# Performance work log

Measured on AMD Instinct MI355X. Metric: run time of the kernel, lower is better.

Reference implementation:

```python
import jax, jax.numpy as jnp
import numpy as np

B, S, D = 4, 2048, 1024

def setup_inputs() -> dict:
    key = jax.random.key(0)
    k0, k1, k2, k3, k4, k5 = jax.random.split(key, 6)
    scale = 1.0 / np.sqrt(D)
    return {
        "input_seq_embs": jax.random.normal(k0, (B, S, D), dtype=jnp.float32),
        "W_Q": jax.random.normal(k1, (D, D), dtype=jnp.float32) * scale,
        "W_K": jax.random.normal(k2, (D, D), dtype=jnp.float32) * scale,
        "W_V": jax.random.normal(k3, (D, D), dtype=jnp.float32) * scale,
        "W_O": jax.random.normal(k4, (D, D), dtype=jnp.float32) * scale,
        "b_O": jax.random.normal(k5, (D,), dtype=jnp.float32) * 0.01,
    }

def reference(input_seq_embs, W_Q, W_K, W_V, W_O, b_O):
    # torch nn.Linear: y = x @ W.T
    Q = jnp.einsum('bsd,ed->bse', input_seq_embs, W_Q)
    K = jnp.einsum('bsd,ed->bse', input_seq_embs, W_K)
    V = jnp.einsum('bsd,ed->bse', input_seq_embs, W_V)
    # NOTE: no 1/sqrt(d) scaling in the original module
    A = jnp.einsum('bqd,bkd->bqk', Q, K)  # [B,S,S]
    # log(tril(ones)) == 0 on/below diagonal, -inf above
    causal = jnp.tril(jnp.ones((S, S), dtype=bool))
    A = jnp.where(causal[None, :, :], A, -jnp.inf)
    A = jax.nn.softmax(A, axis=-1)
    # dropout layers are identity in eval mode
    out = jnp.einsum('bqk,bkd->bqd', A, V)
    out = jnp.einsum('bsd,ed->bse', out, W_O) + b_O
    return out
```

## Files before the change

kernel.cpp:

```cpp
#include <hip/hip_runtime.h>
#include <cstdint>

typedef _Float16 f16x8 __attribute__((ext_vector_type(8)));
typedef _Float16 f16x4 __attribute__((ext_vector_type(4)));
typedef float    f32x4 __attribute__((ext_vector_type(4)));

#define AS1 __attribute__((address_space(1)))
#define AS3 __attribute__((address_space(3)))

__device__ __forceinline__ void load16_lds(const void* g, void* l) {
  __builtin_amdgcn_global_load_lds((AS1 void*)g, (AS3 void*)l, 16, 0, 0);
}

__global__ __launch_bounds__(256) void cvt_all(
    const float* __restrict__ x, const float* __restrict__ wq,
    const float* __restrict__ wk, const float* __restrict__ wv,
    const float* __restrict__ wo,
    _Float16* __restrict__ xh, _Float16* __restrict__ wcat,
    _Float16* __restrict__ woh) {
  long long g = (long long)blockIdx.x * 256 + threadIdx.x;
  const float* in; _Float16* out; long long idx;
  if (g < 2097152)      { in = x;  out = xh;             idx = g; }
  else if (g < 2359296) { in = wq; out = wcat;           idx = g - 2097152; }
  else if (g < 2621440) { in = wk; out = wcat + 1048576; idx = g - 2359296; }
  else if (g < 2883584) { in = wv; out = wcat + 2097152; idx = g - 2621440; }
  else                  { in = wo; out = woh;            idx = g - 2883584; }
  float4 v = ((const float4*)in)[idx];
  f16x4 o;
  o[0] = (_Float16)v.x; o[1] = (_Float16)v.y; o[2] = (_Float16)v.z; o[3] = (_Float16)v.w;
  ((f16x4*)out)[idx] = o;
}

__global__ __launch_bounds__(256) void softmax_causal(float* __restrict__ Sbuf) {
  int g = blockIdx.x;
  int row = g & 2047;
  float* srow = Sbuf + (size_t)g * 2048;
  _Float16* prow = (_Float16*)srow + 2048;
  int L = row + 1;
  int L4 = L & ~3;
  int Lp = ((row >> 7) + 1) << 7;
  int t = threadIdx.x;
  int lane = t & 63, w = t >> 6;

  const float4* s4 = (const float4*)srow;
  float4 v[2];
  int cnt = 0;
  float mx = -3.0e38f;
  for (int j4 = t; j4 * 4 < L4; j4 += 256) {
    float4 q = s4[j4];
    v[cnt++] = q;
    mx = fmaxf(mx, fmaxf(fmaxf(q.x, q.y), fmaxf(q.z, q.w)));
  }
  int jt = L4 + t;
  float tailv = 0.f;
  bool hasTail = (jt < L);
  if (hasTail) { tailv = srow[jt]; mx = fmaxf(mx, tailv); }

  __shared__ float sm[8];
  #pragma unroll
  for (int off = 32; off > 0; off >>= 1) mx = fmaxf(mx, __shfl_down(mx, off));
  if (lane == 0) sm[w] = mx;
  __syncthreads();
  if (t == 0) { float m2 = sm[0]; for (int q = 1; q < 4; q++) m2 = fmaxf(m2, sm[q]); sm[0] = m2; }
  __syncthreads();
  mx = sm[0];

  float sum = 0.f;
  for (int c = 0; c < cnt; c++) {
    v[c].x = __expf(v[c].x - mx); v[c].y = __expf(v[c].y - mx);
    v[c].z = __expf(v[c].z - mx); v[c].w = __expf(v[c].w - mx);
    sum += (v[c].x + v[c].y) + (v[c].z + v[c].w);
  }
  float te = 0.f;
  if (hasTail) { te = __expf(tailv - mx); sum += te; }
  #pragma unroll
  for (int off = 32; off > 0; off >>= 1) sum += __shfl_down(sum, off);
  if (lane == 0) sm[4 + w] = sum;
  __syncthreads();
  if (t == 0) sm[4] = 1.0f / (sm[4] + sm[5] + sm[6] + sm[7]);
  __syncthreads();
  float inv = sm[4];

  f16x4* p4 = (f16x4*)prow;
  cnt = 0;
  for (int j4 = t; j4 * 4 < L4; j4 += 256) {
    float4 q = v[cnt++];
    f16x4 o;
    o[0] = (_Float16)(q.x * inv); o[1] = (_Float16)(q.y * inv);
    o[2] = (_Float16)(q.z * inv); o[3] = (_Float16)(q.w * inv);
    p4[j4] = o;
  }
  if (hasTail) prow[jt] = (_Float16)(te * inv);
  for (int j = L + t; j < Lp; j += 256) prow[j] = (_Float16)0.0f;
}

template <int OUTMODE, bool CAUSAL_SKIP>
__global__ __launch_bounds__(256) void gemm_bt(
    const _Float16* __restrict__ A, const _Float16* __restrict__ B,
    void* __restrict__ Cv, const float* __restrict__ bias,
    int K, int lda, int ldb, int ldc,
    long long aBatch, long long bBatch, long long cBatch) {
  int bx = blockIdx.x, by = blockIdx.y, bz = blockIdx.z;
  if (CAUSAL_SKIP && bx > by) return;
  const _Float16* Ab = A + (long long)bz * aBatch + (long long)by * 128 * lda;
  const _Float16* Bb = B + (long long)bz * bBatch + (long long)bx * 128 * ldb;

  __shared__ _Float16 lA[128 * 32];
  __shared__ _Float16 lB[128 * 32];

  int tid = threadIdx.x;
  int r0 = tid >> 2;
  int c0 = (tid & 3) * 8;
  const _Float16* ga0 = Ab + (long long)r0 * lda + c0;
  const _Float16* ga1 = Ab + (long long)(r0 + 64) * lda + c0;
  const _Float16* gb0 = Bb + (long long)r0 * ldb + c0;
  const _Float16* gb1 = Bb + (long long)(r0 + 64) * ldb + c0;
  _Float16* la0 = lA + tid * 8;
  _Float16* la1 = lA + 2048 + tid * 8;
  _Float16* lb0 = lB + tid * 8;
  _Float16* lb1 = lB + 2048 + tid * 8;

  f32x4 acc[4][4] = {};
  int lane = tid & 63;
  int wv = tid >> 6;
  int wm = (wv & 1) * 64, wn = (wv >> 1) * 64;
  int l16 = lane & 15, quad = lane >> 4;
  const _Float16* raBase = lA + (wm + l16) * 32 + quad * 8;
  const _Float16* rbBase = lB + (wn + l16) * 32 + quad * 8;

  for (int kb = 0; kb < K; kb += 32) {
    __syncthreads();
    load16_lds(ga0, la0);
    load16_lds(ga1, la1);
    load16_lds(gb0, lb0);
    load16_lds(gb1, lb1);
    ga0 += 32; ga1 += 32; gb0 += 32; gb1 += 32;
    __syncthreads();
    f16x8 af[4], bfr[4];
    #pragma unroll
    for (int i = 0; i < 4; i++) af[i] = *(const f16x8*)(raBase + i * 512);
    #pragma unroll
    for (int j = 0; j < 4; j++) bfr[j] = *(const f16x8*)(rbBase + j * 512);
    #pragma unroll
    for (int i = 0; i < 4; i++)
      #pragma unroll
      for (int j = 0; j < 4; j++)
        acc[i][j] = __builtin_amdgcn_mfma_f32_16x16x32_f16(af[i], bfr[j], acc[i][j], 0, 0, 0);
  }

  int m0 = by * 128 + wm + quad * 4;
  int n0 = bx * 128 + wn + l16;

  if (OUTMODE == 2) {
    float* C = (float*)Cv + (long long)bz * cBatch;
    #pragma unroll
    for (int i = 0; i < 4; i++)
      #pragma unroll
      for (int j = 0; j < 4; j++)
        #pragma unroll
        for (int r = 0; r < 4; r++)
          C[(long long)(m0 + i * 16 + r) * ldc + (n0 + j * 16)] = acc[i][j][r];
  } else {
    float* C = (float*)Cv + (long long)bz * cBatch;
    #pragma unroll
    for (int j = 0; j < 4; j++) {
      float bj = bias[n0 + j * 16];
      #pragma unroll
      for (int i = 0; i < 4; i++)
        #pragma unroll
        for (int r = 0; r < 4; r++)
          C[(long long)(m0 + i * 16 + r) * ldc + (n0 + j * 16)] = acc[i][j][r] + bj;
    }
  }
}

__global__ __launch_bounds__(256) void qkv_gemm(
    const _Float16* __restrict__ A, const _Float16* __restrict__ B,
    _Float16* __restrict__ Qh, _Float16* __restrict__ Kh, _Float16* __restrict__ Vt) {
  int bx = blockIdx.x, by = blockIdx.y;
  const _Float16* Ab = A + (long long)by * 128 * 1024;
  const _Float16* Bb = B + (long long)bx * 128 * 1024;

  __shared__ _Float16 lA[128 * 32];
  __shared__ _Float16 lB[128 * 32];

  int tid = threadIdx.x;
  int r0 = tid >> 2;
  int c0 = (tid & 3) * 8;
  const _Float16* ga0 = Ab + (long long)r0 * 1024 + c0;
  const _Float16* ga1 = Ab + (long long)(r0 + 64) * 1024 + c0;
  const _Float16* gb0 = Bb + (long long)r0 * 1024 + c0;
  const _Float16* gb1 = Bb + (long long)(r0 + 64) * 1024 + c0;
  _Float16* la0 = lA + tid * 8;
  _Float16* la1 = lA + 2048 + tid * 8;
  _Float16* lb0 = lB + tid * 8;
  _Float16* lb1 = lB + 2048 + tid * 8;

  f32x4 acc[4][4] = {};
  int lane = tid & 63;
  int wv = tid >> 6;
  int wm = (wv & 1) * 64, wn = (wv >> 1) * 64;
  int l16 = lane & 15, quad = lane >> 4;
  const _Float16* raBase = lA + (wm + l16) * 32 + quad * 8;
  const _Float16* rbBase = lB + (wn + l16) * 32 + quad * 8;

  for (int kb = 0; kb < 1024; kb += 32) {
    __syncthreads();
    load16_lds(ga0, la0);
    load16_lds(ga1, la1);
    load16_lds(gb0, lb0);
    load16_lds(gb1, lb1);
    ga0 += 32; ga1 += 32; gb0 += 32; gb1 += 32;
    __syncthreads();
    f16x8 af[4], bfr[4];
    #pragma unroll
    for (int i = 0; i < 4; i++) af[i] = *(const f16x8*)(raBase + i * 512);
    #pragma unroll
    for (int j = 0; j < 4; j++) bfr[j] = *(const f16x8*)(rbBase + j * 512);
    #pragma unroll
    for (int i = 0; i < 4; i++)
      #pragma unroll
      for (int j = 0; j < 4; j++)
        acc[i][j] = __builtin_amdgcn_mfma_f32_16x16x32_f16(af[i], bfr[j], acc[i][j], 0, 0, 0);
  }

  int m0 = by * 128 + wm + quad * 4;
  int n0 = bx * 128 + wn + l16;

  if (bx < 16) {
    _Float16* C = (bx < 8) ? Qh : Kh;
    int nr = n0 & 1023;
    #pragma unroll
    for (int i = 0; i < 4; i++)
      #pragma unroll
      for (int j = 0; j < 4; j++)
        #pragma unroll
        for (int r = 0; r < 4; r++)
          C[(long long)(m0 + i * 16 + r) * 1024 + (nr + j * 16)] = (_Float16)acc[i][j][r];
  } else {
    int d0 = n0 - 2048;
    #pragma unroll
    for (int i = 0; i < 4; i++) {
      long long mm = m0 + i * 16;
      long long b = mm >> 11;
      long long s = mm & 2047;
      #pragma unroll
      for (int j = 0; j < 4; j++) {
        f16x4 pk;
        #pragma unroll
        for (int r = 0; r < 4; r++) pk[r] = (_Float16)acc[i][j][r];
        *(f16x4*)(Vt + (b << 21) + (long long)(d0 + j * 16) * 2048 + s) = pk;
      }
    }
  }
}

__global__ __launch_bounds__(256) void pv_splitk(
    const _Float16* __restrict__ P,
    const _Float16* __restrict__ Vt,
    float* __restrict__ P0, float* __restrict__ P1,
    _Float16* __restrict__ Oh) {
  int bx = blockIdx.x, cy = blockIdx.y, bz = blockIdx.z;
  int by, c;
  if (cy < 8) { by = cy; c = 0; }
  else { int q = cy - 8; by = 8 + (q >> 1); c = q & 1; }
  int kmax = (by + 1) * 128;
  int k0 = c * 1024;
  int klen = min(kmax, k0 + 1024) - k0;

  const _Float16* Ab = P + (long long)bz * 8388608LL + (long long)by * 128 * 4096 + k0;
  const _Float16* Bb = Vt + (long long)bz * 2097152LL + (long long)bx * 128 * 2048 + k0;

  __shared__ _Float16 lA[128 * 32];
  __shared__ _Float16 lB[128 * 32];

  int tid = threadIdx.x;
  int r0 = tid >> 2;
  int c0 = (tid & 3) * 8;
  const _Float16* ga0 = Ab + (long long)r0 * 4096 + c0;
  const _Float16* ga1 = Ab + (long long)(r0 + 64) * 4096 + c0;
  const _Float16* gb0 = Bb + (long long)r0 * 2048 + c0;
  const _Float16* gb1 = Bb + (long long)(r0 + 64) * 2048 + c0;
  _Float16* la0 = lA + tid * 8;
  _Float16* la1 = lA + 2048 + tid * 8;
  _Float16* lb0 = lB + tid * 8;
  _Float16* lb1 = lB + 2048 + tid * 8;

  f32x4 acc[4][4] = {};
  int lane = tid & 63;
  int wv = tid >> 6;
  int wm = (wv & 1) * 64, wn = (wv >> 1) * 64;
  int l16 = lane & 15, quad = lane >> 4;
  const _Float16* raBase = lA + (wm + l16) * 32 + quad * 8;
  const _Float16* rbBase = lB + (wn + l16) * 32 + quad * 8;

  for (int kb = 0; kb < klen; kb += 32) {
    __syncthreads();
    load16_lds(ga0, la0);
    load16_lds(ga1, la1);
    load16_lds(gb0, lb0);
    load16_lds(gb1, lb1);
    ga0 += 32; ga1 += 32; gb0 += 32; gb1 += 32;
    __syncthreads();
    f16x8 af[4], bfr[4];
    #pragma unroll
    for (int i = 0; i < 4; i++) af[i] = *(const f16x8*)(raBase + i * 512);
    #pragma unroll
    for (int j = 0; j < 4; j++) bfr[j] = *(const f16x8*)(rbBase + j * 512);
    #pragma unroll
    for (int i = 0; i < 4; i++)
      #pragma unroll
      for (int j = 0; j < 4; j++)
        acc[i][j] = __builtin_amdgcn_mfma_f32_16x16x32_f16(af[i], bfr[j], acc[i][j], 0, 0, 0);
  }

  int m0 = by * 128 + wm + quad * 4;
  int n0 = bx * 128 + wn + l16;

  if (c == 0 && by < 8) {
    _Float16* C = Oh + (long long)bz * 2097152LL;
    #pragma unroll
    for (int i = 0; i < 4; i++)
      #pragma unroll
      for (int j = 0; j < 4; j++)
        #pragma unroll
        for (int r = 0; r < 4; r++)
          C[(long long)(m0 + i * 16 + r) * 1024 + (n0 + j * 16)] = (_Float16)acc[i][j][r];
  } else if (c == 0) {
    float* C = P0 + (long long)bz * 2097152LL;
    #pragma unroll
    for (int i = 0; i < 4; i++)
      #pragma unroll
      for (int j = 0; j < 4; j++)
        #pragma unroll
        for (int r = 0; r < 4; r++)
          C[(long long)(m0 + i * 16 + r) * 1024 + (n0 + j * 16)] = acc[i][j][r];
  } else {
    float* C = P1 + (long long)bz * 1048576LL;
    int mr = m0 - 1024;
    #pragma unroll
    for (int i = 0; i < 4; i++)
      #pragma unroll
      for (int j = 0; j < 4; j++)
        #pragma unroll
        for (int r = 0; r < 4; r++)
          C[(long long)(mr + i * 16 + r) * 1024 + (n0 + j * 16)] = acc[i][j][r];
  }
}

__global__ __launch_bounds__(256) void pv_reduce(const float* __restrict__ P0,
                                                 const float* __restrict__ P1,
                                                 _Float16* __restrict__ Oh) {
  int i = blockIdx.x * 256 + threadIdx.x;
  if (i >= 1048576) return;
  int f4 = i;
  int bz = f4 >> 18;
  int loc = f4 & 262143;
  long long p0i = (long long)bz * 524288 + 262144 + loc;
  float4 v = ((const float4*)P0)[p0i];
  float4 w = ((const float4*)P1)[f4];
  v.x += w.x; v.y += w.y; v.z += w.z; v.w += w.w;
  f16x4 o;
  o[0] = (_Float16)v.x; o[1] = (_Float16)v.y; o[2] = (_Float16)v.z; o[3] = (_Float16)v.w;
  ((f16x4*)Oh)[p0i] = o;
}


extern "C" void kernel_launch(void* const* d_in, const int* in_sizes, int n_in,
                              void* d_out, int out_size, void* d_ws, size_t ws_size,
                              hipStream_t stream) {
  const float* x  = (const float*)d_in[0];
  const float* Wq = (const float*)d_in[1];
  const float* Wk = (const float*)d_in[2];
  const float* Wv = (const float*)d_in[3];
  const float* Wo = (const float*)d_in[4];
  const float* bO = (const float*)d_in[5];

  char* ws = (char*)d_ws;
  _Float16* xh   = (_Float16*)(ws + 0);
  _Float16* Wcat = (_Float16*)(ws + 16777216);
  _Float16* Woh  = (_Float16*)(ws + 23068672);
  _Float16* Qh   = (_Float16*)(ws + 25165824);
  _Float16* Kh   = (_Float16*)(ws + 41943040);
  _Float16* Vt   = (_Float16*)(ws + 58720256);
  _Float16* Oh   = (_Float16*)(ws + 75497472);
  float*    Sb   = (float*)   (ws + 92274688);
  float*    P0   = (float*)   (ws + 25165824);
  float*    P1   = (float*)   (ws + 0);

  dim3 blk(256);

  cvt_all<<<12288, blk, 0, stream>>>(x, Wq, Wk, Wv, Wo, xh, Wcat, Woh);

  qkv_gemm<<<dim3(24, 64, 1), blk, 0, stream>>>(xh, Wcat, Qh, Kh, Vt);

  gemm_bt<2, true><<<dim3(16, 16, 4), blk, 0, stream>>>(
      Qh, Kh, Sb, nullptr, 1024, 1024, 1024, 2048,
      2097152LL, 2097152LL, 4194304LL);

  softmax_causal<<<8192, blk, 0, stream>>>(Sb);

  pv_splitk<<<dim3(8, 24, 4), blk, 0, stream>>>(
      (const _Float16*)Sb + 2048, Vt, P0, P1, Oh);
  pv_reduce<<<4096, blk, 0, stream>>>(P0, P1, Oh);

  gemm_bt<3, false><<<dim3(8, 64, 1), blk, 0, stream>>>(
      Oh, Woh, (float*)d_out, bO, 1024, 1024, 1024, 1024, 0, 0, 0);
}
```

Before: 340.3 us.

## Fuse per-tile softmax stats into scores GEMM and store fp16 scores

The scores GEMM now computes per-tile row max and exp-sum in its epilogue, writes fp16 max-shifted scores plus per-tile (max, sum) stats, and a lighter normalize pass rescales the scores into probabilities in place. This replaces the fp32 score buffer and the full-row softmax kernel, cutting the score traffic from fp32 to fp16 and removing the separate max/sum reduction passes. The trade-offs are extra epilogue work and shared-memory reductions in the GEMM, plus precision loss from storing shifted scores in fp16 before exponentiation. The generic gemm_bt template is split into a dedicated output-projection kernel.

```diff
diff --git a/kernel.cpp b/kernel.cpp
--- a/kernel.cpp
+++ b/kernel.cpp
@@ -31,149 +31,6 @@
   ((f16x4*)out)[idx] = o;
 }
 
-__global__ __launch_bounds__(256) void softmax_causal(float* __restrict__ Sbuf) {
-  int g = blockIdx.x;
-  int row = g & 2047;
-  float* srow = Sbuf + (size_t)g * 2048;
-  _Float16* prow = (_Float16*)srow + 2048;
-  int L = row + 1;
-  int L4 = L & ~3;
-  int Lp = ((row >> 7) + 1) << 7;
-  int t = threadIdx.x;
-  int lane = t & 63, w = t >> 6;
-
-  const float4* s4 = (const float4*)srow;
-  float4 v[2];
-  int cnt = 0;
-  float mx = -3.0e38f;
-  for (int j4 = t; j4 * 4 < L4; j4 += 256) {
-    float4 q = s4[j4];
-    v[cnt++] = q;
-    mx = fmaxf(mx, fmaxf(fmaxf(q.x, q.y), fmaxf(q.z, q.w)));
-  }
-  int jt = L4 + t;
-  float tailv = 0.f;
-  bool hasTail = (jt < L);
-  if (hasTail) { tailv = srow[jt]; mx = fmaxf(mx, tailv); }
-
-  __shared__ float sm[8];
-  #pragma unroll
-  for (int off = 32; off > 0; off >>= 1) mx = fmaxf(mx, __shfl_down(mx, off));
-  if (lane == 0) sm[w] = mx;
-  __syncthreads();
-  if (t == 0) { float m2 = sm[0]; for (int q = 1; q < 4; q++) m2 = fmaxf(m2, sm[q]); sm[0] = m2; }
-  __syncthreads();
-  mx = sm[0];
-
-  float sum = 0.f;
-  for (int c = 0; c < cnt; c++) {
-    v[c].x = __expf(v[c].x - mx); v[c].y = __expf(v[c].y - mx);
-    v[c].z = __expf(v[c].z - mx); v[c].w = __expf(v[c].w - mx);
-    sum += (v[c].x + v[c].y) + (v[c].z + v[c].w);
-  }
-  float te = 0.f;
-  if (hasTail) { te = __expf(tailv - mx); sum += te; }
-  #pragma unroll
-  for (int off = 32; off > 0; off >>= 1) sum += __shfl_down(sum, off);
-  if (lane == 0) sm[4 + w] = sum;
-  __syncthreads();
-  if (t == 0) sm[4] = 1.0f / (sm[4] + sm[5] + sm[6] + sm[7]);
-  __syncthreads();
-  float inv = sm[4];
-
-  f16x4* p4 = (f16x4*)prow;
-  cnt = 0;
-  for (int j4 = t; j4 * 4 < L4; j4 += 256) {
-    float4 q = v[cnt++];
-    f16x4 o;
-    o[0] = (_Float16)(q.x * inv); o[1] = (_Float16)(q.y * inv);
-    o[2] = (_Float16)(q.z * inv); o[3] = (_Float16)(q.w * inv);
-    p4[j4] = o;
-  }
-  if (hasTail) prow[jt] = (_Float16)(te * inv);
-  for (int j = L + t; j < Lp; j += 256) prow[j] = (_Float16)0.0f;
-}
-
-template <int OUTMODE, bool CAUSAL_SKIP>
-__global__ __launch_bounds__(256) void gemm_bt(
-    const _Float16* __restrict__ A, const _Float16* __restrict__ B,
-    void* __restrict__ Cv, const float* __restrict__ bias,
-    int K, int lda, int ldb, int ldc,
-    long long aBatch, long long bBatch, long long cBatch) {
-  int bx = blockIdx.x, by = blockIdx.y, bz = blockIdx.z;
-  if (CAUSAL_SKIP && bx > by) return;
-  const _Float16* Ab = A + (long long)bz * aBatch + (long long)by * 128 * lda;
-  const _Float16* Bb = B + (long long)bz * bBatch + (long long)bx * 128 * ldb;
-
-  __shared__ _Float16 lA[128 * 32];
-  __shared__ _Float16 lB[128 * 32];
-
-  int tid = threadIdx.x;
-  int r0 = tid >> 2;
-  int c0 = (tid & 3) * 8;
-  const _Float16* ga0 = Ab + (long long)r0 * lda + c0;
-  const _Float16* ga1 = Ab + (long long)(r0 + 64) * lda + c0;
-  const _Float16* gb0 = Bb + (long long)r0 * ldb + c0;
-  const _Float16* gb1 = Bb + (long long)(r0 + 64) * ldb + c0;
-  _Float16* la0 = lA + tid * 8;
-  _Float16* la1 = lA + 2048 + tid * 8;
-  _Float16* lb0 = lB + tid * 8;
-  _Float16* lb1 = lB + 2048 + tid * 8;
-
-  f32x4 acc[4][4] = {};
-  int lane = tid & 63;
-  int wv = tid >> 6;
-  int wm = (wv & 1) * 64, wn = (wv >> 1) * 64;
-  int l16 = lane & 15, quad = lane >> 4;
-  const _Float16* raBase = lA + (wm + l16) * 32 + quad * 8;
-  const _Float16* rbBase = lB + (wn + l16) * 32 + quad * 8;
-
-  for (int kb = 0; kb < K; kb += 32) {
-    __syncthreads();
-    load16_lds(ga0, la0);
-    load16_lds(ga1, la1);
-    load16_lds(gb0, lb0);
-    load16_lds(gb1, lb1);
-    ga0 += 32; ga1 += 32; gb0 += 32; gb1 += 32;
-    __syncthreads();
-    f16x8 af[4], bfr[4];
-    #pragma unroll
-    for (int i = 0; i < 4; i++) af[i] = *(const f16x8*)(raBase + i * 512);
-    #pragma unroll
-    for (int j = 0; j < 4; j++) bfr[j] = *(const f16x8*)(rbBase + j * 512);
-    #pragma unroll
-    for (int i = 0; i < 4; i++)
-      #pragma unroll
-      for (int j = 0; j < 4; j++)
-        acc[i][j] = __builtin_amdgcn_mfma_f32_16x16x32_f16(af[i], bfr[j], acc[i][j], 0, 0, 0);
-  }
-
-  int m0 = by * 128 + wm + quad * 4;
-  int n0 = bx * 128 + wn + l16;
-
-  if (OUTMODE == 2) {
-    float* C = (float*)Cv + (long long)bz * cBatch;
-    #pragma unroll
-    for (int i = 0; i < 4; i++)
-      #pragma unroll
-      for (int j = 0; j < 4; j++)
-        #pragma unroll
-        for (int r = 0; r < 4; r++)
-          C[(long long)(m0 + i * 16 + r) * ldc + (n0 + j * 16)] = acc[i][j][r];
-  } else {
-    float* C = (float*)Cv + (long long)bz * cBatch;
-    #pragma unroll
-    for (int j = 0; j < 4; j++) {
-      float bj = bias[n0 + j * 16];
-      #pragma unroll
-      for (int i = 0; i < 4; i++)
-        #pragma unroll
-        for (int r = 0; r < 4; r++)
-          C[(long long)(m0 + i * 16 + r) * ldc + (n0 + j * 16)] = acc[i][j][r] + bj;
-    }
-  }
-}
-
 __global__ __launch_bounds__(256) void qkv_gemm(
     const _Float16* __restrict__ A, const _Float16* __restrict__ B,
     _Float16* __restrict__ Qh, _Float16* __restrict__ Kh, _Float16* __restrict__ Vt) {
@@ -252,6 +109,195 @@
         *(f16x4*)(Vt + (b << 21) + (long long)(d0 + j * 16) * 2048 + s) = pk;
       }
     }
+  }
+}
+
+__global__ __launch_bounds__(256) void scores_gemm(
+    const _Float16* __restrict__ Qh, const _Float16* __restrict__ Kh,
+    _Float16* __restrict__ S, float2* __restrict__ stats) {
+  int bx = blockIdx.x, by = blockIdx.y, bz = blockIdx.z;
+  if (bx > by) return;
+  const _Float16* Ab = Qh + (long long)bz * 2097152 + (long long)by * 128 * 1024;
+  const _Float16* Bb = Kh + (long long)bz * 2097152 + (long long)bx * 128 * 1024;
+
+  __shared__ _Float16 lA[128 * 32];
+  __shared__ _Float16 lB[128 * 32];
+  __shared__ float redM[128];
+  __shared__ float redL[128];
+
+  int tid = threadIdx.x;
+  int r0 = tid >> 2;
+  int c0 = (tid & 3) * 8;
+  const _Float16* ga0 = Ab + (long long)r0 * 1024 + c0;
+  const _Float16* ga1 = Ab + (long long)(r0 + 64) * 1024 + c0;
+  const _Float16* gb0 = Bb + (long long)r0 * 1024 + c0;
+  const _Float16* gb1 = Bb + (long long)(r0 + 64) * 1024 + c0;
+  _Float16* la0 = lA + tid * 8;
+  _Float16* la1 = lA + 2048 + tid * 8;
+  _Float16* lb0 = lB + tid * 8;
+  _Float16* lb1 = lB + 2048 + tid * 8;
+
+  f32x4 acc[4][4] = {};
+  int lane = tid & 63;
+  int wv = tid >> 6;
+  int wm = (wv & 1) * 64, wn = (wv >> 1) * 64;
+  int l16 = lane & 15, quad = lane >> 4;
+  const _Float16* raBase = lA + (wm + l16) * 32 + quad * 8;
+  const _Float16* rbBase = lB + (wn + l16) * 32 + quad * 8;
+
+  for (int kb = 0; kb < 1024; kb += 32) {
+    __syncthreads();
+    load16_lds(ga0, la0);
+    load16_lds(ga1, la1);
+    load16_lds(gb0, lb0);
+    load16_lds(gb1, lb1);
+    ga0 += 32; ga1 += 32; gb0 += 32; gb1 += 32;
+    __syncthreads();
+    f16x8 af[4], bfr[4];
+    #pragma unroll
+    for (int i = 0; i < 4; i++) af[i] = *(const f16x8*)(raBase + i * 512);
+    #pragma unroll
+    for (int j = 0; j < 4; j++) bfr[j] = *(const f16x8*)(rbBase + j * 512);
+    #pragma unroll
+    for (int i = 0; i < 4; i++)
+      #pragma unroll
+      for (int j = 0; j < 4; j++)
+        acc[i][j] = __builtin_amdgcn_mfma_f32_16x16x32_f16(af[i], bfr[j], acc[i][j], 0, 0, 0);
+  }
+
+  bool diag = (bx == by);
+  int rloc0 = wm + quad * 4;
+  int cloc0 = wn + l16;
+
+  float mloc[4][4];
+  #pragma unroll
+  for (int i = 0; i < 4; i++)
+    #pragma unroll
+    for (int r = 0; r < 4; r++) {
+      float mx = -3.0e38f;
+      #pragma unroll
+      for (int j = 0; j < 4; j++) {
+        bool ok = !diag || (cloc0 + j * 16 <= rloc0 + i * 16 + r);
+        float s = acc[i][j][r];
+        mx = ok ? fmaxf(mx, s) : mx;
+      }
+      #pragma unroll
+      for (int d = 1; d < 16; d <<= 1) mx = fmaxf(mx, __shfl_xor(mx, d));
+      mloc[i][r] = mx;
+    }
+  __syncthreads();
+  if (wn && (lane & 15) == 0) {
+    #pragma unroll
+    for (int i = 0; i < 4; i++)
+      #pragma unroll
+      for (int r = 0; r < 4; r++) redM[rloc0 + i * 16 + r] = mloc[i][r];
+  }
+  __syncthreads();
+  if (!wn) {
+    #pragma unroll
+    for (int i = 0; i < 4; i++)
+      #pragma unroll
+      for (int r = 0; r < 4; r++)
+        mloc[i][r] = fmaxf(mloc[i][r], redM[rloc0 + i * 16 + r]);
+  }
+  __syncthreads();
+  if (!wn && (lane & 15) == 0) {
+    #pragma unroll
+    for (int i = 0; i < 4; i++)
+      #pragma unroll
+      for (int r = 0; r < 4; r++) redM[rloc0 + i * 16 + r] = mloc[i][r];
+  }
+  __syncthreads();
+  float mfin[4][4];
+  #pragma unroll
+  for (int i = 0; i < 4; i++)
+    #pragma unroll
+    for (int r = 0; r < 4; r++) mfin[i][r] = redM[rloc0 + i * 16 + r];
+
+  float lloc[4][4];
+  #pragma unroll
+  for (int i = 0; i < 4; i++)
+    #pragma unroll
+    for (int r = 0; r < 4; r++) {
+      float sum = 0.f;
+      #pragma unroll
+      for (int j = 0; j < 4; j++) {
+        bool ok = !diag || (cloc0 + j * 16 <= rloc0 + i * 16 + r);
+        float e = __expf(acc[i][j][r] - mfin[i][r]);
+        sum += ok ? e : 0.f;
+      }
+      #pragma unroll
+      for (int d = 1; d < 16; d <<= 1) sum += __shfl_xor(sum, d);
+      lloc[i][r] = sum;
+    }
+  if (wn && (lane & 15) == 0) {
+    #pragma unroll
+    for (int i = 0; i < 4; i++)
+      #pragma unroll
+      for (int r = 0; r < 4; r++) redL[rloc0 + i * 16 + r] = lloc[i][r];
+  }
+  __syncthreads();
+  if (!wn && (lane & 15) == 0) {
+    #pragma unroll
+    for (int i = 0; i < 4; i++)
+      #pragma unroll
+      for (int r = 0; r < 4; r++) {
+        int rl = rloc0 + i * 16 + r;
+        float lt = lloc[i][r] + redL[rl];
+        stats[((long long)bz * 2048 + by * 128 + rl) * 16 + bx] =
+            make_float2(mfin[i][r], lt);
+      }
+  }
+
+  _Float16* Sb = S + (long long)bz * 4194304;
+  int m0 = by * 128 + rloc0;
+  int n0 = bx * 128 + cloc0;
+  #pragma unroll
+  for (int i = 0; i < 4; i++)
+    #pragma unroll
+    for (int j = 0; j < 4; j++)
+      #pragma unroll
+      for (int r = 0; r < 4; r++)
+        Sb[(long long)(m0 + i * 16 + r) * 2048 + (n0 + j * 16)] =
+            (_Float16)(acc[i][j][r] - mfin[i][r]);
+}
+
+__global__ __launch_bounds__(256) void normalize_p(_Float16* __restrict__ S,
+                                                   const float2* __restrict__ stats) {
+  int g = blockIdx.x;
+  int bz = g >> 11, row = g & 2047;
+  int nt = (row >> 7) + 1;
+  _Float16* srow = S + ((long long)bz * 2048 + row) * 2048;
+  const float2* st = stats + ((long long)bz * 2048 + row) * 16;
+  __shared__ float sh_invl;
+  __shared__ float shd[16];
+  int t = threadIdx.x;
+  if (t < 16) {
+    float2 p = (t < nt) ? st[t] : make_float2(-3.0e38f, 0.f);
+    float m = p.x;
+    #pragma unroll
+    for (int d = 1; d < 16; d <<= 1) m = fmaxf(m, __shfl_xor(m, d));
+    float term = p.y * __expf(p.x - m);
+    #pragma unroll
+    for (int d = 1; d < 16; d <<= 1) term += __shfl_xor(term, d);
+    shd[t] = p.x - m;
+    if (t == 0) sh_invl = 1.0f / term;
+  }
+  __syncthreads();
+  float invl = sh_invl;
+  int Lp = nt << 7;
+  for (int c = t; (c << 3) < Lp; c += 256) {
+    float dt = shd[c >> 4];
+    f16x8 v = ((f16x8*)srow)[c];
+    f16x8 o;
+    int col0 = c << 3;
+    #pragma unroll
+    for (int e = 0; e < 8; e++) {
+      float u = (float)v[e];
+      float pe = __expf(u + dt) * invl;
+      o[e] = (col0 + e <= row) ? (_Float16)pe : (_Float16)0.f;
+    }
+    ((f16x8*)srow)[c] = o;
   }
 }
 
@@ -268,7 +314,7 @@
   int k0 = c * 1024;
   int klen = min(kmax, k0 + 1024) - k0;
 
-  const _Float16* Ab = P + (long long)bz * 8388608LL + (long long)by * 128 * 4096 + k0;
+  const _Float16* Ab = P + (long long)bz * 4194304LL + (long long)by * 128 * 2048 + k0;
   const _Float16* Bb = Vt + (long long)bz * 2097152LL + (long long)bx * 128 * 2048 + k0;
 
   __shared__ _Float16 lA[128 * 32];
@@ -277,8 +323,8 @@
   int tid = threadIdx.x;
   int r0 = tid >> 2;
   int c0 = (tid & 3) * 8;
-  const _Float16* ga0 = Ab + (long long)r0 * 4096 + c0;
-  const _Float16* ga1 = Ab + (long long)(r0 + 64) * 4096 + c0;
+  const _Float16* ga0 = Ab + (long long)r0 * 2048 + c0;
+  const _Float16* ga1 = Ab + (long long)(r0 + 64) * 2048 + c0;
   const _Float16* gb0 = Bb + (long long)r0 * 2048 + c0;
   const _Float16* gb1 = Bb + (long long)(r0 + 64) * 2048 + c0;
   _Float16* la0 = lA + tid * 8;
@@ -365,6 +411,69 @@
   ((f16x4*)Oh)[p0i] = o;
 }
 
+__global__ __launch_bounds__(256) void oproj_gemm(
+    const _Float16* __restrict__ A, const _Float16* __restrict__ B,
+    float* __restrict__ C, const float* __restrict__ bias) {
+  int bx = blockIdx.x, by = blockIdx.y;
+  const _Float16* Ab = A + (long long)by * 128 * 1024;
+  const _Float16* Bb = B + (long long)bx * 128 * 1024;
+
+  __shared__ _Float16 lA[128 * 32];
+  __shared__ _Float16 lB[128 * 32];
+
+  int tid = threadIdx.x;
+  int r0 = tid >> 2;
+  int c0 = (tid & 3) * 8;
+  const _Float16* ga0 = Ab + (long long)r0 * 1024 + c0;
+  const _Float16* ga1 = Ab + (long long)(r0 + 64) * 1024 + c0;
+  const _Float16* gb0 = Bb + (long long)r0 * 1024 + c0;
+  const _Float16* gb1 = Bb + (long long)(r0 + 64) * 1024 + c0;
+  _Float16* la0 = lA + tid * 8;
+  _Float16* la1 = lA + 2048 + tid * 8;
+  _Float16* lb0 = lB + tid * 8;
+  _Float16* lb1 = lB + 2048 + tid * 8;
+
+  f32x4 acc[4][4] = {};
+  int lane = tid & 63;
+  int wv = tid >> 6;
+  int wm = (wv & 1) * 64, wn = (wv >> 1) * 64;
+  int l16 = lane & 15, quad = lane >> 4;
+  const _Float16* raBase = lA + (wm + l16) * 32 + quad * 8;
+  const _Float16* rbBase = lB + (wn + l16) * 32 + quad * 8;
+
+  for (int kb = 0; kb < 1024; kb += 32) {
+    __syncthreads();
+    load16_lds(ga0, la0);
+    load16_lds(ga1, la1);
+    load16_lds(gb0, lb0);
+    load16_lds(gb1, lb1);
+    ga0 += 32; ga1 += 32; gb0 += 32; gb1 += 32;
+    __syncthreads();
+    f16x8 af[4], bfr[4];
+    #pragma unroll
+    for (int i = 0; i < 4; i++) af[i] = *(const f16x8*)(raBase + i * 512);
+    #pragma unroll
+    for (int j = 0; j < 4; j++) bfr[j] = *(const f16x8*)(rbBase + j * 512);
+    #pragma unroll
+    for (int i = 0; i < 4; i++)
+      #pragma unroll
+      for (int j = 0; j < 4; j++)
+        acc[i][j] = __builtin_amdgcn_mfma_f32_16x16x32_f16(af[i], bfr[j], acc[i][j], 0, 0, 0);
+  }
+
+  int m0 = by * 128 + wm + quad * 4;
+  int n0 = bx * 128 + wn + l16;
+  #pragma unroll
+  for (int j = 0; j < 4; j++) {
+    float bj = bias[n0 + j * 16];
+    #pragma unroll
+    for (int i = 0; i < 4; i++)
+      #pragma unroll
+      for (int r = 0; r < 4; r++)
+        C[(long long)(m0 + i * 16 + r) * 1024 + (n0 + j * 16)] = acc[i][j][r] + bj;
+  }
+}
+
 
 extern "C" void kernel_launch(void* const* d_in, const int* in_sizes, int n_in,
                               void* d_out, int out_size, void* d_ws, size_t ws_size,
@@ -384,7 +493,8 @@
   _Float16* Kh   = (_Float16*)(ws + 41943040);
   _Float16* Vt   = (_Float16*)(ws + 58720256);
   _Float16* Oh   = (_Float16*)(ws + 75497472);
-  float*    Sb   = (float*)   (ws + 92274688);
+  _Float16* Sb   = (_Float16*)(ws + 92274688);
+  float2*   stats= (float2*)  (ws + 125829120);
   float*    P0   = (float*)   (ws + 25165824);
   float*    P1   = (float*)   (ws + 0);
 
@@ -394,16 +504,12 @@
 
   qkv_gemm<<<dim3(24, 64, 1), blk, 0, stream>>>(xh, Wcat, Qh, Kh, Vt);
 
-  gemm_bt<2, true><<<dim3(16, 16, 4), blk, 0, stream>>>(
-      Qh, Kh, Sb, nullptr, 1024, 1024, 1024, 2048,
-      2097152LL, 2097152LL, 4194304LL);
-
-  softmax_causal<<<8192, blk, 0, stream>>>(Sb);
-
-  pv_splitk<<<dim3(8, 24, 4), blk, 0, stream>>>(
-      (const _Float16*)Sb + 2048, Vt, P0, P1, Oh);
+  scores_gemm<<<dim3(16, 16, 4), blk, 0, stream>>>(Qh, Kh, Sb, stats);
+
+  normalize_p<<<8192, blk, 0, stream>>>(Sb, stats);
+
+  pv_splitk<<<dim3(8, 24, 4), blk, 0, stream>>>(Sb, Vt, P0, P1, Oh);
   pv_reduce<<<4096, blk, 0, stream>>>(P0, P1, Oh);
 
-  gemm_bt<3, false><<<dim3(8, 64, 1), blk, 0, stream>>>(
-      Oh, Woh, (float*)d_out, bO, 1024, 1024, 1024, 1024, 0, 0, 0);
-}
+  oproj_gemm<<<dim3(8, 64, 1), blk, 0, stream>>>(Oh, Woh, (float*)d_out, bO);
+}
```

Measured after the change: 306.4 us. 10.0% less time.
